# Optimization experiments

Hardware: AMD Instinct MI355X
Metric: run time of the kernel (lower is better)

The kernel has to match this reference:

```python
import jax, jax.numpy as jnp
import numpy as np

D_MODEL = 1024
H = 16
D_K = D_MODEL // H
THETA = 10000.0
MAX_SEQ = 2048
SEQ = 2048
BATCH = 2


def _rope_tables():
    # tri[i, k] angles: i / theta**(2k/d_k)
    pos = jnp.arange(MAX_SEQ, dtype=jnp.float32)[:, None]          # [S, 1]
    inv_freq = THETA ** (-2.0 * jnp.arange(D_K // 2, dtype=jnp.float32) / D_K)  # [dk/2]
    ang = pos * inv_freq                                            # [S, dk/2]
    return jnp.cos(ang), jnp.sin(ang)


def _apply_rope(x, token_positions, cos_t, sin_t):
    # x: [b, h, s, dk]; rotate interleaved pairs
    cos = cos_t[token_positions]  # [s, dk/2]
    sin = sin_t[token_positions]
    x2 = x.reshape(x.shape[:-1] + (D_K // 2, 2))
    x0, x1 = x2[..., 0], x2[..., 1]
    r0 = x0 * cos - x1 * sin
    r1 = x0 * sin + x1 * cos
    return jnp.stack([r0, r1], axis=-1).reshape(x.shape)


def setup_inputs() -> dict:
    key = jax.random.key(0)
    ks = jax.random.split(key, 5)
    sigma = np.sqrt(2.0 / (D_MODEL + D_MODEL))
    return {
        "x": jax.random.normal(ks[0], (BATCH, SEQ, D_MODEL), dtype=jnp.float32),
        "token_positions": jnp.arange(SEQ, dtype=jnp.int64 if jax.config.jax_enable_x64 else jnp.int32),
        "Wq": (jax.random.normal(ks[1], (D_MODEL, D_MODEL), dtype=jnp.float32) * sigma),
        "Wk": (jax.random.normal(ks[2], (D_MODEL, D_MODEL), dtype=jnp.float32) * sigma),
        "Wv": (jax.random.normal(ks[3], (D_MODEL, D_MODEL), dtype=jnp.float32) * sigma),
        "Wo": (jax.random.normal(ks[4], (D_MODEL, D_MODEL), dtype=jnp.float32) * sigma),
    }


def reference(x, token_positions, Wq, Wk, Wv, Wo):
    b, s, _ = x.shape
    cos_t, sin_t = _rope_tables()

    def proj(W):
        y = jnp.einsum('oi,bsi->bso', W, x)                 # [b, s, d_model]
        return y.reshape(b, s, H, D_K).transpose(0, 2, 1, 3)  # [b, h, s, dk]

    Q = _apply_rope(proj(Wq), token_positions, cos_t, sin_t)
    K = _apply_rope(proj(Wk), token_positions, cos_t, sin_t)
    V = proj(Wv)

    scores = jnp.einsum('bhqd,bhkd->bhqk', Q, K) / jnp.sqrt(jnp.float32(D_K))
    causal = jnp.tril(jnp.ones((s, s), dtype=bool))
    scores = jnp.where(causal, scores, -jnp.inf)
    attn = jax.nn.softmax(scores, axis=-1)
    out = jnp.einsum('bhqk,bhkd->bhqd', attn, V)            # [b, h, s, dv]
    out = out.transpose(0, 2, 1, 3).reshape(b, s, D_MODEL)
    return jnp.einsum('oi,bsi->bso', Wo, out)
```

## Files before the change

kernel.cpp:

```cpp
#include <hip/hip_runtime.h>
#include <hip/hip_bf16.h>
#include <math.h>

#define D_MODEL 1024
#define NH      16
#define DK      64
#define SEQ     2048
#define BATCH   2

typedef float  f32x4  __attribute__((ext_vector_type(4)));
typedef __bf16 bf16x8 __attribute__((ext_vector_type(8)));
typedef unsigned short ushx4 __attribute__((ext_vector_type(4)));
typedef unsigned short ushx8 __attribute__((ext_vector_type(8)));
typedef unsigned short u16;

__device__ inline u16 cbf(float f) { __bf16 h = (__bf16)f; return *(u16*)&h; }

__device__ inline void gload16(const u16* g, u16* l) {
    __builtin_amdgcn_global_load_lds(
        (const __attribute__((address_space(1))) unsigned int*)g,
        (__attribute__((address_space(3))) unsigned int*)l,
        16, 0, 0);
}

__global__ void rope_tables_kernel(float2* __restrict__ cs) {
    int i = blockIdx.x * 256 + threadIdx.x;
    int pos = i >> 5, k = i & 31;
    float inv = powf(10000.0f, -2.0f * (float)k / 64.0f);
    float ang = (float)pos * inv;
    cs[i] = make_float2(cosf(ang), sinf(ang));
}

__global__ void cvt_kernel(const float* __restrict__ in, u16* __restrict__ out) {
    size_t i = ((size_t)blockIdx.x * 256 + threadIdx.x) * 8;
    f32x4 v0 = *(const f32x4*)(in + i);
    f32x4 v1 = *(const f32x4*)(in + i + 4);
    ushx4 o0, o1;
    #pragma unroll
    for (int e = 0; e < 4; e++) { o0[e] = cbf(v0[e]); o1[e] = cbf(v1[e]); }
    *(ushx4*)(out + i) = o0;
    *(ushx4*)(out + i + 4) = o1;
}

__global__ void cvtw_kernel(const float* __restrict__ wq, const float* __restrict__ wk,
                            const float* __restrict__ wv, const float* __restrict__ wo,
                            u16* __restrict__ oq, u16* __restrict__ ok,
                            u16* __restrict__ ov, u16* __restrict__ oo) {
    const float* in; u16* out;
    switch (blockIdx.y) {
        case 0: in = wq; out = oq; break;
        case 1: in = wk; out = ok; break;
        case 2: in = wv; out = ov; break;
        default: in = wo; out = oo; break;
    }
    size_t i = ((size_t)blockIdx.x * 256 + threadIdx.x) * 8;
    f32x4 v0 = *(const f32x4*)(in + i);
    f32x4 v1 = *(const f32x4*)(in + i + 4);
    ushx4 o0, o1;
    #pragma unroll
    for (int e = 0; e < 4; e++) { o0[e] = cbf(v0[e]); o1[e] = cbf(v1[e]); }
    *(ushx4*)(out + i) = o0;
    *(ushx4*)(out + i + 4) = o1;
}

template<int MODE>
__global__ __launch_bounds__(256) void gemm_bt(
    const u16* __restrict__ A, const u16* __restrict__ W,
    u16* __restrict__ Qo, u16* __restrict__ Ko, void* __restrict__ Oo,
    const int* __restrict__ tpos, const float2* __restrict__ cs)
{
    constexpr int K = 1024;
    __shared__ u16 As[2][128 * 32];
    __shared__ u16 Bs[2][128 * 32];

    const int t  = threadIdx.x;
    const int m0 = blockIdx.x * 128, n0 = blockIdx.y * 128;
    const int lane = t & 63, wid = t >> 6;
    const int wm = wid >> 1, wn = wid & 1;
    const int lr = lane & 15, lg = lane >> 4;

    const int ldrow0 = wid * 32 + (lane >> 2);
    const int ldrow1 = ldrow0 + 16;
    const int lc = lane & 3;
    const u16* Asrc0 = A + (size_t)(m0 + ldrow0) * K + ((lc ^ ((ldrow0 >> 1) & 3)) << 3);
    const u16* Asrc1 = A + (size_t)(m0 + ldrow1) * K + ((lc ^ ((ldrow1 >> 1) & 3)) << 3);
    const u16* Bsrc0 = W + (size_t)(n0 + ldrow0) * K + ((lc ^ ((ldrow0 >> 1) & 3)) << 3);
    const u16* Bsrc1 = W + (size_t)(n0 + ldrow1) * K + ((lc ^ ((ldrow1 >> 1) & 3)) << 3);
    const int d0 = (wid * 32) * 32, d1 = (wid * 32 + 16) * 32;

    f32x4 acc[4][4];
    #pragma unroll
    for (int i = 0; i < 4; i++)
        #pragma unroll
        for (int j2 = 0; j2 < 4; j2++) acc[i][j2] = 0.0f;

    auto stage = [&](int buf, int k0) {
        gload16(Asrc0 + k0, &As[buf][d0]);
        gload16(Asrc1 + k0, &As[buf][d1]);
        gload16(Bsrc0 + k0, &Bs[buf][d0]);
        gload16(Bsrc1 + k0, &Bs[buf][d1]);
    };

    stage(0, 0);
    int buf = 0;
    for (int k0 = 0; k0 < K; k0 += 32) {
        __syncthreads();
        if (k0 + 32 < K) stage(buf ^ 1, k0 + 32);

        bf16x8 af[4], bfr[4];
        #pragma unroll
        for (int mi = 0; mi < 4; mi++) {
            int row = wm * 64 + mi * 16 + lr;
            af[mi] = *(const bf16x8*)&As[buf][row * 32 + ((lg ^ ((row >> 1) & 3)) << 3)];
        }
        #pragma unroll
        for (int ni = 0; ni < 4; ni++) {
            int row = wn * 64 + ni * 16 + lr;
            bfr[ni] = *(const bf16x8*)&Bs[buf][row * 32 + ((lg ^ ((row >> 1) & 3)) << 3)];
        }
        #pragma unroll
        for (int mi = 0; mi < 4; mi++)
            #pragma unroll
            for (int ni = 0; ni < 4; ni++) {
                if constexpr (MODE == 3)
                    acc[mi][ni] = __builtin_amdgcn_mfma_f32_16x16x32_bf16(bfr[ni], af[mi], acc[mi][ni], 0, 0, 0);
                else
                    acc[mi][ni] = __builtin_amdgcn_mfma_f32_16x16x32_bf16(af[mi], bfr[ni], acc[mi][ni], 0, 0, 0);
            }
        buf ^= 1;
    }

    #pragma unroll
    for (int mi = 0; mi < 4; mi++)
        #pragma unroll
        for (int ni = 0; ni < 4; ni++) {
            f32x4 v4 = acc[mi][ni];
            #pragma unroll
            for (int r = 0; r < 4; r++) {
                float v = v4[r];
                if constexpr (MODE == 3) {
                    int n = n0 + wn * 64 + ni * 16 + lg * 4 + r;
                    int m = m0 + wm * 64 + mi * 16 + lr;
                    int h = n >> 6, d = n & 63;
                    int b = m >> 11, s = m & 2047;
                    ((u16*)Oo)[(((size_t)b * NH + h) * DK + d) * SEQ + s] = cbf(v);
                } else {
                    int m = m0 + wm * 64 + mi * 16 + lg * 4 + r;
                    int n = n0 + wn * 64 + ni * 16 + lr;
                    if constexpr (MODE == 2) {
                        ((float*)Oo)[(size_t)m * D_MODEL + n] = v;
                    } else {
                        int b = m >> 11, s = m & 2047;
                        int h = (n >> 6) & 15, d = n & 63;
                        float vp = __shfl_xor(v, 1);
                        int tp = tpos[s];
                        float2 c2 = cs[tp * 32 + (d >> 1)];
                        float res = (d & 1) ? (vp * c2.y + v * c2.x) : (v * c2.x - vp * c2.y);
                        const int sel = n0 >> 10;
                        if (sel == 0) res *= 0.18033688f;
                        u16* outp = sel ? Ko : Qo;
                        outp[(((size_t)b * NH + h) * SEQ + s) * DK + d] = cbf(res);
                    }
                }
            }
        }
}

__global__ __launch_bounds__(256) void attn_kernel(
    const u16* __restrict__ Q,
    const u16* __restrict__ Km,
    const u16* __restrict__ VT,
    u16* __restrict__ aout)
{
    __shared__ u16 Ks[2][64 * 64];
    __shared__ u16 Vs[64 * 64];
    __shared__ u16 Pl[4][16 * 64];
    const int t = threadIdx.x, wid = t >> 6, lane = t & 63;
    const int lr = lane & 15, lg = lane >> 4;
    const int bx = blockIdx.x;
    const int j = bx & 31;
    const int p = bx >> 5;
    const int bh = (j & 7) * 4 + (j >> 3);
    const int b = bh >> 4, h = bh & 15;
    const int srow = lane >> 3, schunk = lane & 7;
    const int row0 = wid * 16;
    const int swz = (schunk ^ srow) << 3;

    const u16* Qg = Q  + (size_t)bh * SEQ * DK;
    const u16* Kg = Km + (size_t)bh * SEQ * DK;
    const u16* Vg = VT + (size_t)bh * DK * SEQ;
    u16* Plw = Pl[wid];

    auto process = [&](int qb) {
        const int q0 = qb * 64;
        const int qw = q0 + row0;
        const int nkt = qb + 1;

        __syncthreads();

        bf16x8 aq[2];
        #pragma unroll
        for (int h2 = 0; h2 < 2; h2++)
            aq[h2] = *(const bf16x8*)&Qg[(qw + lr) * DK + h2 * 32 + lg * 8];

        float m_run = -__builtin_inff(), l_run = 0.0f;
        f32x4 acc[4];
        #pragma unroll
        for (int dg = 0; dg < 4; dg++) acc[dg] = 0.0f;

        const u16* kptr = Kg + (size_t)(row0 + srow) * DK + swz;
        const u16* vptr = Vg + (size_t)(row0 + srow) * SEQ + swz;

        gload16(kptr,          &Ks[0][row0 * 64]);
        gload16(kptr + 8 * DK, &Ks[0][(row0 + 8) * 64]);
        kptr += 64 * DK;

        for (int kt = 0; kt < nkt; kt++) {
            __builtin_amdgcn_sched_barrier(0);
            __builtin_amdgcn_s_barrier();
            __builtin_amdgcn_sched_barrier(0);
            gload16(vptr,                   &Vs[row0 * 64]);
            gload16(vptr + (size_t)8 * SEQ, &Vs[(row0 + 8) * 64]);
            vptr += 64;
            u16* kd = &Ks[(kt + 1) & 1][0];
            gload16(kptr,          kd + row0 * 64);
            gload16(kptr + 8 * DK, kd + (row0 + 8) * 64);
            kptr += 64 * DK;
            const int kb = kt * 64;

            asm volatile("s_waitcnt vmcnt(4)" ::: "memory");
            __builtin_amdgcn_sched_barrier(0);
            bf16x8 kf[4][2];
            #pragma unroll
            for (int kg = 0; kg < 4; kg++)
                #pragma unroll
                for (int h2 = 0; h2 < 2; h2++) {
                    int row = kg * 16 + lr;
                    kf[kg][h2] = *(const bf16x8*)&Ks[kt & 1][row * 64 + (((h2 * 4 + lg) ^ (lr & 7)) << 3)];
                }

            f32x4 sf[4];
            #pragma unroll
            for (int kg = 0; kg < 4; kg++) sf[kg] = 0.0f;
            __builtin_amdgcn_s_setprio(1);
            #pragma unroll
            for (int kg = 0; kg < 4; kg++) {
                sf[kg] = __builtin_amdgcn_mfma_f32_16x16x32_bf16(kf[kg][0], aq[0], sf[kg], 0, 0, 0);
                sf[kg] = __builtin_amdgcn_mfma_f32_16x16x32_bf16(kf[kg][1], aq[1], sf[kg], 0, 0, 0);
            }
            __builtin_amdgcn_s_setprio(0);

            {
                if (kb + 64 > qw) {
                    const int qq = qw + lr;
                    #pragma unroll
                    for (int kg = 0; kg < 4; kg++)
                        #pragma unroll
                        for (int r = 0; r < 4; r++)
                            if (kb + kg * 16 + lg * 4 + r > qq) sf[kg][r] = -__builtin_inff();
                }
                float cmax = sf[0][0];
                #pragma unroll
                for (int kg = 0; kg < 4; kg++)
                    #pragma unroll
                    for (int r = 0; r < 4; r++) cmax = fmaxf(cmax, sf[kg][r]);
                if (!__all(cmax <= m_run + 8.0f)) {
                    float mt = fmaxf(cmax, __shfl_xor(cmax, 16));
                    mt = fmaxf(mt, __shfl_xor(mt, 32));
                    float mn = fmaxf(m_run, mt);
                    float scr = exp2f(m_run - mn);
                    m_run = mn;
                    l_run *= scr;
                    #pragma unroll
                    for (int dg = 0; dg < 4; dg++) acc[dg] *= scr;
                }
                float l = 0.0f;
                const int prow = lr * 64;
                #pragma unroll
                for (int kg = 0; kg < 4; kg++) {
                    ushx4 pk;
                    #pragma unroll
                    for (int r = 0; r < 4; r++) {
                        float pv = exp2f(sf[kg][r] - m_run);
                        l += pv;
                        pk[r] = cbf(pv);
                    }
                    *(ushx4*)&Plw[prow + (((kg * 4 + lg) ^ ((lr & 7) << 1)) << 2)] = pk;
                }
                l_run += l;
            }

            asm volatile("s_waitcnt vmcnt(2)" ::: "memory");
            __builtin_amdgcn_sched_barrier(0);
            bf16x8 vf[2][4];
            #pragma unroll
            for (int ck = 0; ck < 2; ck++)
                #pragma unroll
                for (int dg = 0; dg < 4; dg++) {
                    int row = dg * 16 + lr;
                    vf[ck][dg] = *(const bf16x8*)&Vs[row * 64 + (((ck * 4 + lg) ^ (lr & 7)) << 3)];
                }

            asm volatile("s_waitcnt lgkmcnt(0)" ::: "memory");
            __builtin_amdgcn_sched_barrier(0);
            bf16x8 pa[2];
            #pragma unroll
            for (int ck = 0; ck < 2; ck++)
                pa[ck] = *(const bf16x8*)&Plw[lr * 64 + (((ck * 8 + lg * 2) ^ ((lr & 7) << 1)) << 2)];
            __builtin_amdgcn_s_setprio(1);
            #pragma unroll
            for (int ck = 0; ck < 2; ck++)
                #pragma unroll
                for (int dg = 0; dg < 4; dg++)
                    acc[dg] = __builtin_amdgcn_mfma_f32_16x16x32_bf16(vf[ck][dg], pa[ck], acc[dg], 0, 0, 0);
            __builtin_amdgcn_s_setprio(0);
        }

        l_run += __shfl_xor(l_run, 16);
        l_run += __shfl_xor(l_run, 32);

        {
            float inv = 1.0f / l_run;
            int q = qw + lr;
            #pragma unroll
            for (int dg = 0; dg < 4; dg++) {
                ushx4 ow;
                #pragma unroll
                for (int r = 0; r < 4; r++) ow[r] = cbf(acc[dg][r] * inv);
                *(ushx4*)&aout[((size_t)b * SEQ + q) * D_MODEL + h * DK + dg * 16 + lg * 4] = ow;
            }
        }
    };

    process(31 - p);
    process(p);
}

extern "C" void kernel_launch(void* const* d_in, const int* in_sizes, int n_in,
                              void* d_out, int out_size, void* d_ws, size_t ws_size,
                              hipStream_t stream) {
    const float* x    = (const float*)d_in[0];
    const int*   tpos = (const int*)d_in[1];
    const float* Wq   = (const float*)d_in[2];
    const float* Wk   = (const float*)d_in[3];
    const float* Wv   = (const float*)d_in[4];
    const float* Wo   = (const float*)d_in[5];
    float* out = (float*)d_out;

    char* ws = (char*)d_ws;
    float2* cs = (float2*)ws;
    u16* Qb   = (u16*)(ws + (512 << 10));
    u16* Kb   = (u16*)(ws + (512 << 10) + ((size_t)8  << 20));
    u16* VT   = (u16*)(ws + (512 << 10) + ((size_t)16 << 20));
    u16* xb   = (u16*)(ws + (512 << 10) + ((size_t)24 << 20));
    u16* Wqb  = (u16*)(ws + (512 << 10) + ((size_t)32 << 20));
    u16* Wkb  = (u16*)(ws + (512 << 10) + ((size_t)34 << 20));
    u16* Wvb  = (u16*)(ws + (512 << 10) + ((size_t)36 << 20));
    u16* Wob  = (u16*)(ws + (512 << 10) + ((size_t)38 << 20));
    u16* attnb = xb;

    rope_tables_kernel<<<256, 256, 0, stream>>>(cs);
    cvt_kernel<<<2048, 256, 0, stream>>>(x, xb);
    cvtw_kernel<<<dim3(512, 4), 256, 0, stream>>>(Wq, Wk, Wv, Wo, Wqb, Wkb, Wvb, Wob);

    gemm_bt<0><<<dim3(32, 16), 256, 0, stream>>>(xb, Wqb, Qb, Kb, nullptr, tpos, cs);
    gemm_bt<3><<<dim3(32, 8),  256, 0, stream>>>(xb, Wvb, nullptr, nullptr, VT, tpos, cs);

    attn_kernel<<<512, 256, 0, stream>>>(Qb, Kb, VT, attnb);

    gemm_bt<2><<<dim3(32, 8),  256, 0, stream>>>(attnb, Wob, nullptr, nullptr, out, tpos, cs);
}
```

Before: 134.1 us.

## Fuse QKV projection launches, split attention blocks per q-tile, narrow out-proj tiles

Q, K and V projections now run in a single launch over contiguous bf16 weights, with a per-block branch selecting the V-transpose epilogue. Attention launches one block per query tile instead of pairing tiles, using a reordered tile mapping for balance, and computes the softmax denominator with an extra MFMA against a ones vector instead of scalar adds. The output projection uses 128x64 tiles for more blocks. These changes aim to cut launch count and raise occupancy, but they rely on Wq, Wk and Wv being laid out contiguously in the workspace and add per-block imbalance in attention.

Result: slower. 171.1 us (+27.6%).

```diff
diff --git a/kernel.cpp b/kernel.cpp
--- a/kernel.cpp
+++ b/kernel.cpp
@@ -63,10 +63,9 @@
     *(ushx4*)(out + i + 4) = o1;
 }
 
-template<int MODE>
-__global__ __launch_bounds__(256) void gemm_bt(
-    const u16* __restrict__ A, const u16* __restrict__ W,
-    u16* __restrict__ Qo, u16* __restrict__ Ko, void* __restrict__ Oo,
+__global__ __launch_bounds__(256) void gemm_qkv(
+    const u16* __restrict__ A, const u16* __restrict__ Wqkv,
+    u16* __restrict__ Qo, u16* __restrict__ Ko, u16* __restrict__ Vo,
     const int* __restrict__ tpos, const float2* __restrict__ cs)
 {
     constexpr int K = 1024;
@@ -78,14 +77,15 @@
     const int lane = t & 63, wid = t >> 6;
     const int wm = wid >> 1, wn = wid & 1;
     const int lr = lane & 15, lg = lane >> 4;
+    const int sel = n0 >> 10;
 
     const int ldrow0 = wid * 32 + (lane >> 2);
     const int ldrow1 = ldrow0 + 16;
     const int lc = lane & 3;
-    const u16* Asrc0 = A + (size_t)(m0 + ldrow0) * K + ((lc ^ ((ldrow0 >> 1) & 3)) << 3);
-    const u16* Asrc1 = A + (size_t)(m0 + ldrow1) * K + ((lc ^ ((ldrow1 >> 1) & 3)) << 3);
-    const u16* Bsrc0 = W + (size_t)(n0 + ldrow0) * K + ((lc ^ ((ldrow0 >> 1) & 3)) << 3);
-    const u16* Bsrc1 = W + (size_t)(n0 + ldrow1) * K + ((lc ^ ((ldrow1 >> 1) & 3)) << 3);
+    const u16* Asrc0 = A    + (size_t)(m0 + ldrow0) * K + ((lc ^ ((ldrow0 >> 1) & 3)) << 3);
+    const u16* Asrc1 = A    + (size_t)(m0 + ldrow1) * K + ((lc ^ ((ldrow1 >> 1) & 3)) << 3);
+    const u16* Bsrc0 = Wqkv + (size_t)(n0 + ldrow0) * K + ((lc ^ ((ldrow0 >> 1) & 3)) << 3);
+    const u16* Bsrc1 = Wqkv + (size_t)(n0 + ldrow1) * K + ((lc ^ ((ldrow1 >> 1) & 3)) << 3);
     const int d0 = (wid * 32) * 32, d1 = (wid * 32 + 16) * 32;
 
     f32x4 acc[4][4];
@@ -118,15 +118,19 @@
             int row = wn * 64 + ni * 16 + lr;
             bfr[ni] = *(const bf16x8*)&Bs[buf][row * 32 + ((lg ^ ((row >> 1) & 3)) << 3)];
         }
-        #pragma unroll
-        for (int mi = 0; mi < 4; mi++)
-            #pragma unroll
-            for (int ni = 0; ni < 4; ni++) {
-                if constexpr (MODE == 3)
+        if (sel == 2) {
+            #pragma unroll
+            for (int mi = 0; mi < 4; mi++)
+                #pragma unroll
+                for (int ni = 0; ni < 4; ni++)
                     acc[mi][ni] = __builtin_amdgcn_mfma_f32_16x16x32_bf16(bfr[ni], af[mi], acc[mi][ni], 0, 0, 0);
-                else
+        } else {
+            #pragma unroll
+            for (int mi = 0; mi < 4; mi++)
+                #pragma unroll
+                for (int ni = 0; ni < 4; ni++)
                     acc[mi][ni] = __builtin_amdgcn_mfma_f32_16x16x32_bf16(af[mi], bfr[ni], acc[mi][ni], 0, 0, 0);
-            }
+        }
         buf ^= 1;
     }
 
@@ -138,30 +142,98 @@
             #pragma unroll
             for (int r = 0; r < 4; r++) {
                 float v = v4[r];
-                if constexpr (MODE == 3) {
+                if (sel == 2) {
                     int n = n0 + wn * 64 + ni * 16 + lg * 4 + r;
                     int m = m0 + wm * 64 + mi * 16 + lr;
-                    int h = n >> 6, d = n & 63;
+                    int h = (n >> 6) & 15, d = n & 63;
                     int b = m >> 11, s = m & 2047;
-                    ((u16*)Oo)[(((size_t)b * NH + h) * DK + d) * SEQ + s] = cbf(v);
+                    Vo[(((size_t)b * NH + h) * DK + d) * SEQ + s] = cbf(v);
                 } else {
                     int m = m0 + wm * 64 + mi * 16 + lg * 4 + r;
                     int n = n0 + wn * 64 + ni * 16 + lr;
-                    if constexpr (MODE == 2) {
-                        ((float*)Oo)[(size_t)m * D_MODEL + n] = v;
-                    } else {
-                        int b = m >> 11, s = m & 2047;
-                        int h = (n >> 6) & 15, d = n & 63;
-                        float vp = __shfl_xor(v, 1);
-                        int tp = tpos[s];
-                        float2 c2 = cs[tp * 32 + (d >> 1)];
-                        float res = (d & 1) ? (vp * c2.y + v * c2.x) : (v * c2.x - vp * c2.y);
-                        const int sel = n0 >> 10;
-                        if (sel == 0) res *= 0.18033688f;
-                        u16* outp = sel ? Ko : Qo;
-                        outp[(((size_t)b * NH + h) * SEQ + s) * DK + d] = cbf(res);
-                    }
+                    int b = m >> 11, s = m & 2047;
+                    int h = (n >> 6) & 15, d = n & 63;
+                    float vp = __shfl_xor(v, 1);
+                    int tp = tpos[s];
+                    float2 c2 = cs[tp * 32 + (d >> 1)];
+                    float res = (d & 1) ? (vp * c2.y + v * c2.x) : (v * c2.x - vp * c2.y);
+                    if (sel == 0) res *= 0.18033688f;
+                    u16* outp = sel ? Ko : Qo;
+                    outp[(((size_t)b * NH + h) * SEQ + s) * DK + d] = cbf(res);
                 }
+            }
+        }
+}
+
+__global__ __launch_bounds__(256) void gemm_out(
+    const u16* __restrict__ A, const u16* __restrict__ W, float* __restrict__ outp)
+{
+    constexpr int K = 1024;
+    __shared__ u16 As[2][128 * 32];
+    __shared__ u16 Bs[2][64 * 32];
+
+    const int t  = threadIdx.x;
+    const int m0 = blockIdx.x * 128, n0 = blockIdx.y * 64;
+    const int lane = t & 63, wid = t >> 6;
+    const int wm = wid >> 1, wn = wid & 1;
+    const int lr = lane & 15, lg = lane >> 4;
+
+    const int ldrow0 = wid * 32 + (lane >> 2);
+    const int ldrow1 = ldrow0 + 16;
+    const int lc = lane & 3;
+    const int brow = wid * 16 + (lane >> 2);
+    const u16* Asrc0 = A + (size_t)(m0 + ldrow0) * K + ((lc ^ ((ldrow0 >> 1) & 3)) << 3);
+    const u16* Asrc1 = A + (size_t)(m0 + ldrow1) * K + ((lc ^ ((ldrow1 >> 1) & 3)) << 3);
+    const u16* Bsrc0 = W + (size_t)(n0 + brow) * K + ((lc ^ ((brow >> 1) & 3)) << 3);
+    const int da0 = (wid * 32) * 32, da1 = (wid * 32 + 16) * 32, db0 = (wid * 16) * 32;
+
+    f32x4 acc[4][2];
+    #pragma unroll
+    for (int i = 0; i < 4; i++)
+        #pragma unroll
+        for (int j2 = 0; j2 < 2; j2++) acc[i][j2] = 0.0f;
+
+    auto stage = [&](int buf, int k0) {
+        gload16(Asrc0 + k0, &As[buf][da0]);
+        gload16(Asrc1 + k0, &As[buf][da1]);
+        gload16(Bsrc0 + k0, &Bs[buf][db0]);
+    };
+
+    stage(0, 0);
+    int buf = 0;
+    for (int k0 = 0; k0 < K; k0 += 32) {
+        __syncthreads();
+        if (k0 + 32 < K) stage(buf ^ 1, k0 + 32);
+
+        bf16x8 af[4], bfr[2];
+        #pragma unroll
+        for (int mi = 0; mi < 4; mi++) {
+            int row = wm * 64 + mi * 16 + lr;
+            af[mi] = *(const bf16x8*)&As[buf][row * 32 + ((lg ^ ((row >> 1) & 3)) << 3)];
+        }
+        #pragma unroll
+        for (int ni = 0; ni < 2; ni++) {
+            int row = wn * 32 + ni * 16 + lr;
+            bfr[ni] = *(const bf16x8*)&Bs[buf][row * 32 + ((lg ^ ((row >> 1) & 3)) << 3)];
+        }
+        #pragma unroll
+        for (int mi = 0; mi < 4; mi++)
+            #pragma unroll
+            for (int ni = 0; ni < 2; ni++)
+                acc[mi][ni] = __builtin_amdgcn_mfma_f32_16x16x32_bf16(af[mi], bfr[ni], acc[mi][ni], 0, 0, 0);
+        buf ^= 1;
+    }
+
+    #pragma unroll
+    for (int mi = 0; mi < 4; mi++)
+        #pragma unroll
+        for (int ni = 0; ni < 2; ni++) {
+            f32x4 v4 = acc[mi][ni];
+            #pragma unroll
+            for (int r = 0; r < 4; r++) {
+                int m = m0 + wm * 64 + mi * 16 + lg * 4 + r;
+                int n = n0 + wn * 32 + ni * 16 + lr;
+                outp[(size_t)m * D_MODEL + n] = v4[r];
             }
         }
 }
@@ -179,11 +251,16 @@
     const int lr = lane & 15, lg = lane >> 4;
     const int bx = blockIdx.x;
     const int j = bx & 31;
-    const int p = bx >> 5;
+    const int qidx = bx >> 5;
+    const int gq = qidx >> 3, iq = qidx & 7;
+    const int qb = (gq == 0) ? iq : (gq == 1) ? 15 - iq : (gq == 2) ? 16 + iq : 31 - iq;
     const int bh = (j & 7) * 4 + (j >> 3);
     const int b = bh >> 4, h = bh & 15;
+    const int q0 = qb * 64;
+    const int row0 = wid * 16;
+    const int qw = q0 + row0;
+    const int nkt = qb + 1;
     const int srow = lane >> 3, schunk = lane & 7;
-    const int row0 = wid * 16;
     const int swz = (schunk ^ srow) << 3;
 
     const u16* Qg = Q  + (size_t)bh * SEQ * DK;
@@ -191,149 +268,137 @@
     const u16* Vg = VT + (size_t)bh * DK * SEQ;
     u16* Plw = Pl[wid];
 
-    auto process = [&](int qb) {
-        const int q0 = qb * 64;
-        const int qw = q0 + row0;
-        const int nkt = qb + 1;
-
-        __syncthreads();
-
-        bf16x8 aq[2];
-        #pragma unroll
-        for (int h2 = 0; h2 < 2; h2++)
-            aq[h2] = *(const bf16x8*)&Qg[(qw + lr) * DK + h2 * 32 + lg * 8];
-
-        float m_run = -__builtin_inff(), l_run = 0.0f;
-        f32x4 acc[4];
-        #pragma unroll
-        for (int dg = 0; dg < 4; dg++) acc[dg] = 0.0f;
-
-        const u16* kptr = Kg + (size_t)(row0 + srow) * DK + swz;
-        const u16* vptr = Vg + (size_t)(row0 + srow) * SEQ + swz;
-
-        gload16(kptr,          &Ks[0][row0 * 64]);
-        gload16(kptr + 8 * DK, &Ks[0][(row0 + 8) * 64]);
+    bf16x8 aq[2];
+    #pragma unroll
+    for (int h2 = 0; h2 < 2; h2++)
+        aq[h2] = *(const bf16x8*)&Qg[(qw + lr) * DK + h2 * 32 + lg * 8];
+
+    bf16x8 onesf;
+    #pragma unroll
+    for (int e = 0; e < 8; e++) onesf[e] = (__bf16)1.0f;
+
+    float m_run = -__builtin_inff();
+    f32x4 acc[4];
+    f32x4 acc_l = 0.0f;
+    #pragma unroll
+    for (int dg = 0; dg < 4; dg++) acc[dg] = 0.0f;
+
+    const u16* kptr = Kg + (size_t)(row0 + srow) * DK + swz;
+    const u16* vptr = Vg + (size_t)(row0 + srow) * SEQ + swz;
+
+    gload16(kptr,          &Ks[0][row0 * 64]);
+    gload16(kptr + 8 * DK, &Ks[0][(row0 + 8) * 64]);
+    kptr += 64 * DK;
+
+    for (int kt = 0; kt < nkt; kt++) {
+        __builtin_amdgcn_sched_barrier(0);
+        __builtin_amdgcn_s_barrier();
+        __builtin_amdgcn_sched_barrier(0);
+        gload16(vptr,                   &Vs[row0 * 64]);
+        gload16(vptr + (size_t)8 * SEQ, &Vs[(row0 + 8) * 64]);
+        vptr += 64;
+        u16* kd = &Ks[(kt + 1) & 1][0];
+        gload16(kptr,          kd + row0 * 64);
+        gload16(kptr + 8 * DK, kd + (row0 + 8) * 64);
         kptr += 64 * DK;
-
-        for (int kt = 0; kt < nkt; kt++) {
-            __builtin_amdgcn_sched_barrier(0);
-            __builtin_amdgcn_s_barrier();
-            __builtin_amdgcn_sched_barrier(0);
-            gload16(vptr,                   &Vs[row0 * 64]);
-            gload16(vptr + (size_t)8 * SEQ, &Vs[(row0 + 8) * 64]);
-            vptr += 64;
-            u16* kd = &Ks[(kt + 1) & 1][0];
-            gload16(kptr,          kd + row0 * 64);
-            gload16(kptr + 8 * DK, kd + (row0 + 8) * 64);
-            kptr += 64 * DK;
-            const int kb = kt * 64;
-
-            asm volatile("s_waitcnt vmcnt(4)" ::: "memory");
-            __builtin_amdgcn_sched_barrier(0);
-            bf16x8 kf[4][2];
-            #pragma unroll
-            for (int kg = 0; kg < 4; kg++)
-                #pragma unroll
-                for (int h2 = 0; h2 < 2; h2++) {
-                    int row = kg * 16 + lr;
-                    kf[kg][h2] = *(const bf16x8*)&Ks[kt & 1][row * 64 + (((h2 * 4 + lg) ^ (lr & 7)) << 3)];
-                }
-
-            f32x4 sf[4];
-            #pragma unroll
-            for (int kg = 0; kg < 4; kg++) sf[kg] = 0.0f;
-            __builtin_amdgcn_s_setprio(1);
-            #pragma unroll
-            for (int kg = 0; kg < 4; kg++) {
-                sf[kg] = __builtin_amdgcn_mfma_f32_16x16x32_bf16(kf[kg][0], aq[0], sf[kg], 0, 0, 0);
-                sf[kg] = __builtin_amdgcn_mfma_f32_16x16x32_bf16(kf[kg][1], aq[1], sf[kg], 0, 0, 0);
-            }
-            __builtin_amdgcn_s_setprio(0);
-
-            {
-                if (kb + 64 > qw) {
-                    const int qq = qw + lr;
-                    #pragma unroll
-                    for (int kg = 0; kg < 4; kg++)
-                        #pragma unroll
-                        for (int r = 0; r < 4; r++)
-                            if (kb + kg * 16 + lg * 4 + r > qq) sf[kg][r] = -__builtin_inff();
-                }
-                float cmax = sf[0][0];
+        const int kb = kt * 64;
+
+        asm volatile("s_waitcnt vmcnt(4)" ::: "memory");
+        __builtin_amdgcn_sched_barrier(0);
+        bf16x8 kf[4][2];
+        #pragma unroll
+        for (int kg = 0; kg < 4; kg++)
+            #pragma unroll
+            for (int h2 = 0; h2 < 2; h2++) {
+                int row = kg * 16 + lr;
+                kf[kg][h2] = *(const bf16x8*)&Ks[kt & 1][row * 64 + (((h2 * 4 + lg) ^ (lr & 7)) << 3)];
+            }
+
+        f32x4 sf[4];
+        #pragma unroll
+        for (int kg = 0; kg < 4; kg++) sf[kg] = 0.0f;
+        __builtin_amdgcn_s_setprio(1);
+        #pragma unroll
+        for (int kg = 0; kg < 4; kg++) {
+            sf[kg] = __builtin_amdgcn_mfma_f32_16x16x32_bf16(kf[kg][0], aq[0], sf[kg], 0, 0, 0);
+            sf[kg] = __builtin_amdgcn_mfma_f32_16x16x32_bf16(kf[kg][1], aq[1], sf[kg], 0, 0, 0);
+        }
+        __builtin_amdgcn_s_setprio(0);
+
+        {
+            if (kb + 64 > qw) {
+                const int qq = qw + lr;
                 #pragma unroll
                 for (int kg = 0; kg < 4; kg++)
                     #pragma unroll
-                    for (int r = 0; r < 4; r++) cmax = fmaxf(cmax, sf[kg][r]);
-                if (!__all(cmax <= m_run + 8.0f)) {
-                    float mt = fmaxf(cmax, __shfl_xor(cmax, 16));
-                    mt = fmaxf(mt, __shfl_xor(mt, 32));
-                    float mn = fmaxf(m_run, mt);
-                    float scr = exp2f(m_run - mn);
-                    m_run = mn;
-                    l_run *= scr;
-                    #pragma unroll
-                    for (int dg = 0; dg < 4; dg++) acc[dg] *= scr;
-                }
-                float l = 0.0f;
-                const int prow = lr * 64;
+                    for (int r = 0; r < 4; r++)
+                        if (kb + kg * 16 + lg * 4 + r > qq) sf[kg][r] = -__builtin_inff();
+            }
+            float mk[4];
+            #pragma unroll
+            for (int kg = 0; kg < 4; kg++)
+                mk[kg] = fmaxf(fmaxf(sf[kg][0], sf[kg][1]), fmaxf(sf[kg][2], sf[kg][3]));
+            float cmax = fmaxf(fmaxf(mk[0], mk[1]), fmaxf(mk[2], mk[3]));
+            if (!__all(cmax <= m_run + 8.0f)) {
+                float mt = fmaxf(cmax, __shfl_xor(cmax, 16));
+                mt = fmaxf(mt, __shfl_xor(mt, 32));
+                float mn = fmaxf(m_run, mt);
+                float scr = exp2f(m_run - mn);
+                m_run = mn;
+                acc_l[0] *= scr;
                 #pragma unroll
-                for (int kg = 0; kg < 4; kg++) {
-                    ushx4 pk;
-                    #pragma unroll
-                    for (int r = 0; r < 4; r++) {
-                        float pv = exp2f(sf[kg][r] - m_run);
-                        l += pv;
-                        pk[r] = cbf(pv);
-                    }
-                    *(ushx4*)&Plw[prow + (((kg * 4 + lg) ^ ((lr & 7) << 1)) << 2)] = pk;
-                }
-                l_run += l;
-            }
-
-            asm volatile("s_waitcnt vmcnt(2)" ::: "memory");
-            __builtin_amdgcn_sched_barrier(0);
-            bf16x8 vf[2][4];
-            #pragma unroll
-            for (int ck = 0; ck < 2; ck++)
+                for (int dg = 0; dg < 4; dg++) acc[dg] *= scr;
+            }
+            const int prow = lr * 64;
+            #pragma unroll
+            for (int kg = 0; kg < 4; kg++) {
+                ushx4 pk;
                 #pragma unroll
-                for (int dg = 0; dg < 4; dg++) {
-                    int row = dg * 16 + lr;
-                    vf[ck][dg] = *(const bf16x8*)&Vs[row * 64 + (((ck * 4 + lg) ^ (lr & 7)) << 3)];
-                }
-
-            asm volatile("s_waitcnt lgkmcnt(0)" ::: "memory");
-            __builtin_amdgcn_sched_barrier(0);
-            bf16x8 pa[2];
-            #pragma unroll
-            for (int ck = 0; ck < 2; ck++)
-                pa[ck] = *(const bf16x8*)&Plw[lr * 64 + (((ck * 8 + lg * 2) ^ ((lr & 7) << 1)) << 2)];
-            __builtin_amdgcn_s_setprio(1);
-            #pragma unroll
-            for (int ck = 0; ck < 2; ck++)
-                #pragma unroll
-                for (int dg = 0; dg < 4; dg++)
-                    acc[dg] = __builtin_amdgcn_mfma_f32_16x16x32_bf16(vf[ck][dg], pa[ck], acc[dg], 0, 0, 0);
-            __builtin_amdgcn_s_setprio(0);
-        }
-
-        l_run += __shfl_xor(l_run, 16);
-        l_run += __shfl_xor(l_run, 32);
-
-        {
-            float inv = 1.0f / l_run;
-            int q = qw + lr;
+                for (int r = 0; r < 4; r++)
+                    pk[r] = cbf(exp2f(sf[kg][r] - m_run));
+                *(ushx4*)&Plw[prow + (((kg * 4 + lg) ^ ((lr & 7) << 1)) << 2)] = pk;
+            }
+        }
+
+        asm volatile("s_waitcnt vmcnt(2)" ::: "memory");
+        __builtin_amdgcn_sched_barrier(0);
+        bf16x8 vf[2][4];
+        #pragma unroll
+        for (int ck = 0; ck < 2; ck++)
             #pragma unroll
             for (int dg = 0; dg < 4; dg++) {
-                ushx4 ow;
-                #pragma unroll
-                for (int r = 0; r < 4; r++) ow[r] = cbf(acc[dg][r] * inv);
-                *(ushx4*)&aout[((size_t)b * SEQ + q) * D_MODEL + h * DK + dg * 16 + lg * 4] = ow;
-            }
-        }
-    };
-
-    process(31 - p);
-    process(p);
+                int row = dg * 16 + lr;
+                vf[ck][dg] = *(const bf16x8*)&Vs[row * 64 + (((ck * 4 + lg) ^ (lr & 7)) << 3)];
+            }
+
+        asm volatile("s_waitcnt lgkmcnt(0)" ::: "memory");
+        __builtin_amdgcn_sched_barrier(0);
+        bf16x8 pa[2];
+        #pragma unroll
+        for (int ck = 0; ck < 2; ck++)
+            pa[ck] = *(const bf16x8*)&Plw[lr * 64 + (((ck * 8 + lg * 2) ^ ((lr & 7) << 1)) << 2)];
+        __builtin_amdgcn_s_setprio(1);
+        #pragma unroll
+        for (int ck = 0; ck < 2; ck++) {
+            #pragma unroll
+            for (int dg = 0; dg < 4; dg++)
+                acc[dg] = __builtin_amdgcn_mfma_f32_16x16x32_bf16(vf[ck][dg], pa[ck], acc[dg], 0, 0, 0);
+            acc_l = __builtin_amdgcn_mfma_f32_16x16x32_bf16(onesf, pa[ck], acc_l, 0, 0, 0);
+        }
+        __builtin_amdgcn_s_setprio(0);
+    }
+
+    {
+        float inv = 1.0f / acc_l[0];
+        int q = qw + lr;
+        #pragma unroll
+        for (int dg = 0; dg < 4; dg++) {
+            ushx4 ow;
+            #pragma unroll
+            for (int r = 0; r < 4; r++) ow[r] = cbf(acc[dg][r] * inv);
+            *(ushx4*)&aout[((size_t)b * SEQ + q) * D_MODEL + h * DK + dg * 16 + lg * 4] = ow;
+        }
+    }
 }
 
 extern "C" void kernel_launch(void* const* d_in, const int* in_sizes, int n_in,
@@ -363,10 +428,9 @@
     cvt_kernel<<<2048, 256, 0, stream>>>(x, xb);
     cvtw_kernel<<<dim3(512, 4), 256, 0, stream>>>(Wq, Wk, Wv, Wo, Wqb, Wkb, Wvb, Wob);
 
-    gemm_bt<0><<<dim3(32, 16), 256, 0, stream>>>(xb, Wqb, Qb, Kb, nullptr, tpos, cs);
-    gemm_bt<3><<<dim3(32, 8),  256, 0, stream>>>(xb, Wvb, nullptr, nullptr, VT, tpos, cs);
-
-    attn_kernel<<<512, 256, 0, stream>>>(Qb, Kb, VT, attnb);
-
-    gemm_bt<2><<<dim3(32, 8),  256, 0, stream>>>(attnb, Wob, nullptr, nullptr, out, tpos, cs);
-}
+    gemm_qkv<<<dim3(32, 24), 256, 0, stream>>>(xb, Wqb, Qb, Kb, VT, tpos, cs);
+
+    attn_kernel<<<1024, 256, 0, stream>>>(Qb, Kb, VT, attnb);
+
+    gemm_out<<<dim3(32, 16), 256, 0, stream>>>(attnb, Wob, out);
+}
```
